# Optimization experiments

Hardware: AMD Instinct MI355X
Metric: run time of the kernel (lower is better)

Reference implementation:

```python
import jax, jax.numpy as jnp
import numpy as np

NEG_SLOPE = 0.2  # PyG GATConv default negative_slope
BN_EPS = 1e-5


def gat_layer(x, src, dst, W, b, a_src, a_dst, heads, out_ch, concat):
    # x: [N, Fin]; W: [Fin, heads*out_ch]; a_src/a_dst: [heads, out_ch]
    N = x.shape[0]
    h = (x @ W).reshape(N, heads, out_ch)
    s = (h * a_src).sum(-1)            # [N, H]
    d = (h * a_dst).sum(-1)            # [N, H]
    e = jax.nn.leaky_relu(s[src] + d[dst], NEG_SLOPE)   # [E, H]
    # segment softmax over incoming edges of each destination node
    m = jax.ops.segment_max(e, dst, num_segments=N)
    ex = jnp.exp(e - m[dst])
    denom = jax.ops.segment_sum(ex, dst, num_segments=N)
    alpha = ex / (denom[dst] + 1e-16)                   # [E, H]
    out = jax.ops.segment_sum(alpha[:, :, None] * h[src], dst, num_segments=N)  # [N,H,C]
    out = out.reshape(N, heads * out_ch) if concat else out.mean(axis=1)
    return out + b


def batchnorm(x, gamma, beta):
    mu = x.mean(axis=0)
    var = x.var(axis=0)
    return gamma * (x - mu) * jax.lax.rsqrt(var + BN_EPS) + beta


def setup_inputs() -> dict:
    key = jax.random.key(0)
    ks = jax.random.split(key, 24)
    N, E, Fin, Hd, heads, C = 50000, 800000, 128, 64, 4, 2
    wdim = Hd * heads  # 256
    inp = {
        'x': jax.random.normal(ks[0], (N, Fin), jnp.float32),
        'edge_index': jax.random.randint(ks[1], (2, E), 0, N, jnp.int64),
    }
    def glorot(k, shape):
        fan = shape[0] + shape[-1]
        return jax.random.normal(k, shape, jnp.float32) * np.sqrt(2.0 / fan)
    # layer 0: Fin -> heads x Hd (concat)
    inp['W0'] = glorot(ks[2], (Fin, wdim)); inp['b0'] = jnp.zeros((wdim,), jnp.float32)
    inp['asrc0'] = glorot(ks[3], (heads, Hd)); inp['adst0'] = glorot(ks[4], (heads, Hd))
    inp['g0'] = jnp.ones((wdim,), jnp.float32); inp['be0'] = jnp.zeros((wdim,), jnp.float32)
    # layer 1: wdim -> heads x Hd (concat)
    inp['W1'] = glorot(ks[5], (wdim, wdim)); inp['b1'] = jnp.zeros((wdim,), jnp.float32)
    inp['asrc1'] = glorot(ks[6], (heads, Hd)); inp['adst1'] = glorot(ks[7], (heads, Hd))
    inp['g1'] = jnp.ones((wdim,), jnp.float32); inp['be1'] = jnp.zeros((wdim,), jnp.float32)
    # layer 2: wdim -> 1 head x Hd (no concat)
    inp['W2'] = glorot(ks[8], (wdim, Hd)); inp['b2'] = jnp.zeros((Hd,), jnp.float32)
    inp['asrc2'] = glorot(ks[9], (1, Hd)); inp['adst2'] = glorot(ks[10], (1, Hd))
    inp['g2'] = jnp.ones((Hd,), jnp.float32); inp['be2'] = jnp.zeros((Hd,), jnp.float32)
    # classifier: Linear(2*Hd, Hd) -> ReLU -> Linear(Hd, C)
    inp['Wc1'] = glorot(ks[11], (2 * Hd, Hd)); inp['bc1'] = jnp.zeros((Hd,), jnp.float32)
    inp['Wc2'] = glorot(ks[12], (Hd, C)); inp['bc2'] = jnp.zeros((C,), jnp.float32)
    return inp


def reference(x, edge_index, W0, b0, asrc0, adst0, g0, be0,
              W1, b1, asrc1, adst1, g1, be1,
              W2, b2, asrc2, adst2, g2, be2,
              Wc1, bc1, Wc2, bc2):
    N = x.shape[0]
    # add self-loops (PyG GATConv default)
    loops = jnp.arange(N, dtype=edge_index.dtype)
    src = jnp.concatenate([edge_index[0], loops])
    dst = jnp.concatenate([edge_index[1], loops])
    heads, Hd = asrc0.shape[0], asrc0.shape[1]

    h = gat_layer(x, src, dst, W0, b0, asrc0, adst0, heads, Hd, True)
    h = jax.nn.relu(batchnorm(h, g0, be0))
    h = gat_layer(h, src, dst, W1, b1, asrc1, adst1, heads, Hd, True)
    h = jax.nn.relu(batchnorm(h, g1, be1))
    h = gat_layer(h, src, dst, W2, b2, asrc2, adst2, 1, Hd, False)
    h = jax.nn.relu(batchnorm(h, g2, be2))

    pooled = jnp.concatenate([h.mean(axis=0, keepdims=True),
                              h.max(axis=0, keepdims=True)], axis=1)  # [1, 2*Hd]
    z = jax.nn.relu(pooled @ Wc1 + bc1)
    return z @ Wc2 + bc2  # [1, num_classes]
```

## Files before the change

### kernel.cpp

```cpp
#include <hip/hip_runtime.h>


typedef unsigned int uint;
typedef unsigned short ushort;

#define NEG_SLOPE 0.2f
#define BN_EPS 1e-5f
#define NB_RED 256

typedef __attribute__((ext_vector_type(2))) float f32x2;

__device__ __forceinline__ float bf2f(uint u) { return __uint_as_float(u << 16); }
__device__ __forceinline__ ushort f2bf(float f) {
    uint u = __float_as_uint(f);
    u += 0x7fff + ((u >> 16) & 1);
    return (ushort)(u >> 16);
}


__global__ void prep_kernel(const float* __restrict__ x, ushort* __restrict__ xb,
                            int total_real, int total_pad,
                            const float* __restrict__ W0, ushort* __restrict__ w0t,
                            const float* __restrict__ W1, ushort* __restrict__ w1t,
                            const float* __restrict__ W2, ushort* __restrict__ w2t,
                            const int* __restrict__ ei, int* __restrict__ deg, int E) {
    int i = blockIdx.x * blockDim.x + threadIdx.x;
    if (i < total_pad) {
        xb[i] = (i < total_real) ? f2bf(x[i]) : (ushort)0;
        return;
    }
    int j = i - total_pad;
    if (j < 32768) {
        int n = j / 128, k = j - n * 128;
        w0t[j] = f2bf(W0[(size_t)k * 256 + n]);
        return;
    }
    j -= 32768;
    if (j < 65536) {
        int n = j / 256, k = j - n * 256;
        w1t[j] = f2bf(W1[(size_t)k * 256 + n]);
        return;
    }
    j -= 65536;
    if (j < 16384) {
        int n = j / 256, k = j - n * 256;
        w2t[j] = f2bf(W2[(size_t)k * 64 + n]);
        return;
    }
    j -= 16384;
    if (j < E) atomicAdd(&deg[ei[E + j]], 1);
}


__global__ void scan_part(const int* __restrict__ deg, int* __restrict__ offsets,
                          int* __restrict__ bsum, int N) {
    __shared__ int sh[256];
    int t = threadIdx.x;
    int base = blockIdx.x * 1024 + t * 4;
    int v0 = (base + 0 < N) ? deg[base + 0] : 0;
    int v1 = (base + 1 < N) ? deg[base + 1] : 0;
    int v2 = (base + 2 < N) ? deg[base + 2] : 0;
    int v3 = (base + 3 < N) ? deg[base + 3] : 0;
    int s = v0 + v1 + v2 + v3;
    sh[t] = s;
    __syncthreads();
    for (int off = 1; off < 256; off <<= 1) {
        int y = (t >= off) ? sh[t - off] : 0;
        __syncthreads();
        sh[t] += y;
        __syncthreads();
    }
    int p = sh[t] - s;
    if (base + 0 < N) offsets[base + 0] = p;
    p += v0;
    if (base + 1 < N) offsets[base + 1] = p;
    p += v1;
    if (base + 2 < N) offsets[base + 2] = p;
    p += v2;
    if (base + 3 < N) offsets[base + 3] = p;
    if (t == 255) bsum[blockIdx.x] = sh[255];
}

__global__ void scan_top(const int* __restrict__ bsum, int* __restrict__ bexcl,
                         int nb, int* __restrict__ offsets, int N) {
    if (threadIdx.x == 0) {
        int run = 0;
        for (int b = 0; b < nb; ++b) { bexcl[b] = run; run += bsum[b]; }
        offsets[N] = run;
    }
}

__global__ void scan_add(int* __restrict__ offsets, int* __restrict__ cursor,
                         const int* __restrict__ bexcl, int N) {
    int add = bexcl[blockIdx.x];
    int base = blockIdx.x * 1024 + threadIdx.x * 4;
#pragma unroll
    for (int k = 0; k < 4; ++k) {
        int i = base + k;
        if (i < N) { int v = offsets[i] + add; offsets[i] = v; cursor[i] = v; }
    }
}

__global__ void scatter_kernel(const int* __restrict__ ei, int* __restrict__ cursor,
                               int* __restrict__ srcs, int E) {
    int e = blockIdx.x * blockDim.x + threadIdx.x;
    if (e < E) {
        int s = ei[e];
        int d = ei[E + e];
        int p = atomicAdd(&cursor[d], 1);
        srcs[p] = s;
    }
}


typedef __attribute__((ext_vector_type(8))) short bf16x8;
typedef __attribute__((ext_vector_type(4))) float floatx4;

template <int BN, int H>
__launch_bounds__(256)
__global__ void mfma_gemm_bt(const ushort* __restrict__ A, const ushort* __restrict__ Bt,
                             ushort* __restrict__ C, const float* __restrict__ asrc,
                             const float* __restrict__ adst, float* __restrict__ sv,
                             float* __restrict__ dv, int K, int Nn) {
    constexpr int WCOLS = (BN == 128) ? 2 : 1;
    constexpr int WROWS = 4 / WCOLS;
    constexpr int MT = 128 / (WROWS * 16);
    constexpr int NT = BN / (WCOLS * 16);
    constexpr int BCALLS = (BN * 32 * 2) / 4096;

    __shared__ ushort As[128 * 32];
    __shared__ ushort Bs[BN * 32];

    int t = threadIdx.x;
    int w = t >> 6, l = t & 63;

    int rb, cb;
    if (BN == 128) {
        int nbr = (int)gridDim.x >> 1;
        int full = (nbr & ~7) << 1;
        int id = blockIdx.x;
        if (id < full) {
            rb = ((id >> 4) << 3) + (id & 7);
            cb = (id >> 3) & 1;
        } else {
            int o = id - full;
            int rem = nbr & 7;
            rb = (nbr & ~7) + (rem ? (o % rem) : 0);
            cb = rem ? (o / rem) : 0;
        }
    } else {
        rb = blockIdx.x;
        cb = 0;
    }
    int row0 = rb * 128;
    int col0 = cb * BN;
    int wr = (w / WCOLS) * (MT * 16);
    int wc = (w % WCOLS) * (NT * 16);

    floatx4 acc[MT][NT];
#pragma unroll
    for (int mi = 0; mi < MT; ++mi)
#pragma unroll
        for (int ni = 0; ni < NT; ++ni)
#pragma unroll
            for (int r = 0; r < 4; ++r) acc[mi][ni][r] = 0.f;

    int mrow = l & 15;
    int kc = (l >> 4) * 8;

    for (int kt = 0; kt < K; kt += 32) {
#pragma unroll
        for (int c = 0; c < 2; ++c) {
            int idx = c * 256 + t;
            const ushort* gp = A + (size_t)(row0 + (idx >> 2)) * K + kt + (idx & 3) * 8;
            __builtin_amdgcn_global_load_lds(
                (const __attribute__((address_space(1))) void*)gp,
                (__attribute__((address_space(3))) void*)(As + (idx & ~63) * 8),
                16, 0, 0);
        }
#pragma unroll
        for (int c = 0; c < BCALLS; ++c) {
            int idx = c * 256 + t;
            const ushort* gp = Bt + (size_t)(col0 + (idx >> 2)) * K + kt + (idx & 3) * 8;
            __builtin_amdgcn_global_load_lds(
                (const __attribute__((address_space(1))) void*)gp,
                (__attribute__((address_space(3))) void*)(Bs + (idx & ~63) * 8),
                16, 0, 0);
        }
        __syncthreads();

        bf16x8 af[MT], bfr[NT];
#pragma unroll
        for (int mi = 0; mi < MT; ++mi)
            af[mi] = *(const bf16x8*)&As[(wr + mi * 16 + mrow) * 32 + kc];
#pragma unroll
        for (int ni = 0; ni < NT; ++ni)
            bfr[ni] = *(const bf16x8*)&Bs[(wc + ni * 16 + mrow) * 32 + kc];
#pragma unroll
        for (int mi = 0; mi < MT; ++mi)
#pragma unroll
            for (int ni = 0; ni < NT; ++ni)
                acc[mi][ni] = __builtin_amdgcn_mfma_f32_16x16x32_bf16(
                    af[mi], bfr[ni], acc[mi][ni], 0, 0, 0);
        __syncthreads();
    }

#pragma unroll
    for (int mi = 0; mi < MT; ++mi) {
        int rbase = row0 + wr + mi * 16 + (l >> 4) * 4;
#pragma unroll
        for (int ni = 0; ni < NT; ++ni) {
            int col = col0 + wc + ni * 16 + (l & 15);
#pragma unroll
            for (int r = 0; r < 4; ++r)
                C[(size_t)(rbase + r) * Nn + col] = f2bf(acc[mi][ni][r]);
        }
    }

    float av[NT], bv[NT];
#pragma unroll
    for (int ni = 0; ni < NT; ++ni) {
        int ch = col0 + wc + ni * 16 + (l & 15);
        av[ni] = asrc[ch];
        bv[ni] = adst[ch];
    }
    int gh = (col0 + wc) >> 6;
#pragma unroll
    for (int mi = 0; mi < MT; ++mi) {
#pragma unroll
        for (int r = 0; r < 4; ++r) {
            float s = 0.f, d = 0.f;
#pragma unroll
            for (int ni = 0; ni < NT; ++ni) {
                float hv = acc[mi][ni][r];
                s += hv * av[ni];
                d += hv * bv[ni];
            }
#pragma unroll
            for (int m = 8; m >= 1; m >>= 1) {
                s += __shfl_xor(s, m);
                d += __shfl_xor(d, m);
            }
            if ((l & 15) == 0) {
                int row = row0 + wr + mi * 16 + (l >> 4) * 4 + r;
                sv[row * H + gh] = s;
                dv[row * H + gh] = d;
            }
        }
    }
}


#define CAP4 64

#define ACCUMW4(qv_, wt_) { \
    f32x2 wv_ = {(wt_), (wt_)}; \
    uint pr_[4] = {(qv_).x, (qv_).y, (qv_).z, (qv_).w}; \
    _Pragma("unroll") \
    for (int k_ = 0; k_ < 4; ++k_) { \
        f32x2 hv_ = {__uint_as_float(pr_[k_] << 16), \
                     __uint_as_float(pr_[k_] & 0xffff0000u)}; \
        ax[k_] += wv_ * hv_; \
    } }

#define LDQ4(kk_, wv_, qv_) { \
    int kq_ = (kk_); \
    if (kq_ < scnt) { \
        int nq_ = sidx[sub][kq_]; \
        wv_ = swgt[sub][kq_][head]; \
        qv_ = *(const uint4*)(hrow + (size_t)nq_ * 256); \
    } else { wv_ = 0.f; qv_.x = 0; qv_.y = 0; qv_.z = 0; qv_.w = 0; } }

__launch_bounds__(128)
__global__ void agg4_kernel(const ushort* __restrict__ hb, const float* __restrict__ sv,
                            const float* __restrict__ dv, const int* __restrict__ offsets,
                            const int* __restrict__ srcs, const float* __restrict__ bias,
                            ushort* __restrict__ zb, int N) {
    __shared__ int   sidx[4][CAP4];
    __shared__ float swgt[4][CAP4][4];
    __shared__ float lden[4][4];

    int t = threadIdx.x;
    int sub = t >> 5, gl = t & 31;
    int head = gl >> 3;
    int i = blockIdx.x * 4 + sub;
    bool valid = i < N;

    int beg = 0, cnt = 0;
    if (valid) { beg = offsets[i]; cnt = offsets[i + 1] - beg; }
    int scnt = cnt < CAP4 ? cnt : CAP4;

    if (gl < 4) lden[sub][gl] = 0.f;
    for (int k = gl; k < scnt; k += 32) sidx[sub][k] = srcs[beg + k];
    __syncthreads();

    {
        int h = gl & 3;
        float dvh = valid ? dv[i * 4 + h] : 0.f;
        float denp = 0.f;
        for (int idx = gl; idx < scnt * 4; idx += 32) {
            int k = idx >> 2;
            float e = sv[sidx[sub][k] * 4 + h] + dvh;
            float wgt = __expf(fminf(fmaxf(e, NEG_SLOPE * e), 60.f));
            swgt[sub][k][h] = wgt;
            denp += wgt;
        }
        atomicAdd(&lden[sub][h], denp);
    }
    __syncthreads();

    f32x2 ax[4] = {};
    const ushort* hrow = hb + gl * 8;

    float w0, w1, w2, w3;
    uint4 q0, q1, q2, q3;
    LDQ4(0, w0, q0); LDQ4(1, w1, q1); LDQ4(2, w2, q2); LDQ4(3, w3, q3);
    for (int k = 0; k < scnt; k += 4) {
        float v0 = w0, v1 = w1, v2 = w2, v3 = w3;
        uint4 p0 = q0, p1 = q1, p2 = q2, p3 = q3;
        LDQ4(k + 4, w0, q0); LDQ4(k + 5, w1, q1);
        LDQ4(k + 6, w2, q2); LDQ4(k + 7, w3, q3);
        ACCUMW4(p0, v0);
        ACCUMW4(p1, v1);
        ACCUMW4(p2, v2);
        ACCUMW4(p3, v3);
    }

    if (cnt > CAP4) {
        float d_i = dv[i * 4 + head];
        for (int k2 = CAP4; k2 < cnt; ++k2) {
            int n = srcs[beg + k2];
            float e = sv[n * 4 + head] + d_i;
            float wgt = __expf(fminf(fmaxf(e, NEG_SLOPE * e), 60.f));
            if ((gl & 7) == 0) atomicAdd(&lden[sub][head], wgt);
            uint4 q4 = *(const uint4*)(hrow + (size_t)n * 256);
            ACCUMW4(q4, wgt);
        }
    }

    if (valid) {
        float e_self = sv[i * 4 + head] + dv[i * 4 + head];
        float wself = __expf(fminf(fmaxf(e_self, NEG_SLOPE * e_self), 60.f));
        uint4 qs = *(const uint4*)&hb[(size_t)i * 256 + gl * 8];
        ACCUMW4(qs, wself);
        float rden = 1.f / (lden[sub][head] + wself + 1e-16f);
        const float* bb = bias + gl * 8;
        uint4 o;
        o.x = (uint)f2bf(ax[0].x * rden + bb[0]) | ((uint)f2bf(ax[0].y * rden + bb[1]) << 16);
        o.y = (uint)f2bf(ax[1].x * rden + bb[2]) | ((uint)f2bf(ax[1].y * rden + bb[3]) << 16);
        o.z = (uint)f2bf(ax[2].x * rden + bb[4]) | ((uint)f2bf(ax[2].y * rden + bb[5]) << 16);
        o.w = (uint)f2bf(ax[3].x * rden + bb[6]) | ((uint)f2bf(ax[3].y * rden + bb[7]) << 16);
        *(uint4*)&zb[(size_t)i * 256 + gl * 8] = o;
    }
}


#define CAP1 64

#define ACCUMW1(qv_, wt_) { \
    f32x2 wv_ = {(wt_), (wt_)}; \
    f32x2 h0_ = {__uint_as_float((qv_).x << 16), __uint_as_float((qv_).x & 0xffff0000u)}; \
    f32x2 h1_ = {__uint_as_float((qv_).y << 16), __uint_as_float((qv_).y & 0xffff0000u)}; \
    ax[0] += wv_ * h0_; \
    ax[1] += wv_ * h1_; }

#define LDQ1(kk_, wv_, qv_) { \
    int kq_ = (kk_); \
    if (kq_ < scnt) { \
        int nq_ = sidx[sub][kq_]; \
        wv_ = swgt[sub][kq_]; \
        qv_ = *(const uint2*)(hrow + (size_t)nq_ * 64); \
    } else { wv_ = 0.f; qv_.x = 0; qv_.y = 0; } }

__launch_bounds__(64)
__global__ void agg1_kernel(const ushort* __restrict__ hb, const float* __restrict__ sv,
                            const float* __restrict__ dv, const int* __restrict__ offsets,
                            const int* __restrict__ srcs, const float* __restrict__ bias,
                            ushort* __restrict__ zb, int N) {
    __shared__ int   sidx[4][CAP1];
    __shared__ float swgt[4][CAP1];
    __shared__ float lden[4];

    int t = threadIdx.x;
    int sub = t >> 4, gl = t & 15;
    int i = blockIdx.x * 4 + sub;
    bool valid = i < N;

    int beg = 0, cnt = 0;
    if (valid) { beg = offsets[i]; cnt = offsets[i + 1] - beg; }
    int scnt = cnt < CAP1 ? cnt : CAP1;

    if (gl == 0) lden[sub] = 0.f;
    for (int k = gl; k < scnt; k += 16) sidx[sub][k] = srcs[beg + k];
    __syncthreads();

    float d_i = valid ? dv[i] : 0.f;
    {
        float denp = 0.f;
        for (int k = gl; k < scnt; k += 16) {
            float e = sv[sidx[sub][k]] + d_i;
            float wgt = __expf(fminf(fmaxf(e, NEG_SLOPE * e), 60.f));
            swgt[sub][k] = wgt;
            denp += wgt;
        }
        atomicAdd(&lden[sub], denp);
    }
    __syncthreads();

    f32x2 ax[2] = {};
    const ushort* hrow = hb + gl * 4;

    float w0, w1, w2, w3;
    uint2 q0, q1, q2, q3;
    LDQ1(0, w0, q0); LDQ1(1, w1, q1); LDQ1(2, w2, q2); LDQ1(3, w3, q3);
    for (int k = 0; k < scnt; k += 4) {
        float v0 = w0, v1 = w1, v2 = w2, v3 = w3;
        uint2 p0 = q0, p1 = q1, p2 = q2, p3 = q3;
        LDQ1(k + 4, w0, q0); LDQ1(k + 5, w1, q1);
        LDQ1(k + 6, w2, q2); LDQ1(k + 7, w3, q3);
        ACCUMW1(p0, v0);
        ACCUMW1(p1, v1);
        ACCUMW1(p2, v2);
        ACCUMW1(p3, v3);
    }

    if (cnt > CAP1) {
        for (int k2 = CAP1; k2 < cnt; ++k2) {
            int n = srcs[beg + k2];
            float e = sv[n] + d_i;
            float wgt = __expf(fminf(fmaxf(e, NEG_SLOPE * e), 60.f));
            if (gl == 0) atomicAdd(&lden[sub], wgt);
            uint2 q2v = *(const uint2*)(hrow + (size_t)n * 64);
            ACCUMW1(q2v, wgt);
        }
    }

    if (valid) {
        float e_self = sv[i] + d_i;
        float wself = __expf(fminf(fmaxf(e_self, NEG_SLOPE * e_self), 60.f));
        uint2 qs = *(const uint2*)&hb[(size_t)i * 64 + gl * 4];
        ACCUMW1(qs, wself);
        float rden = 1.f / (lden[sub] + wself + 1e-16f);
        const float* bb = bias + gl * 4;
        uint2 o;
        o.x = (uint)f2bf(ax[0].x * rden + bb[0]) | ((uint)f2bf(ax[0].y * rden + bb[1]) << 16);
        o.y = (uint)f2bf(ax[1].x * rden + bb[2]) | ((uint)f2bf(ax[1].y * rden + bb[3]) << 16);
        *(uint2*)&zb[(size_t)i * 64 + gl * 4] = o;
    }
}


template <int F>
__launch_bounds__(256)
__global__ void bn_stats_kernel(const ushort* __restrict__ x, float* __restrict__ ps,
                                float* __restrict__ pq, int N) {
    constexpr int OCT = F / 8;
    __shared__ float lds_s[F], lds_q[F];
    int t = threadIdx.x;
    if (t < F) { lds_s[t] = 0.f; lds_q[t] = 0.f; }
    __syncthreads();

    float s[8] = {}, q[8] = {};
    int total8 = N * F / 8;
    for (int idx = blockIdx.x * 256 + t; idx < total8; idx += NB_RED * 256) {
        uint4 v = ((const uint4*)x)[idx];
        uint pr[4] = {v.x, v.y, v.z, v.w};
#pragma unroll
        for (int k = 0; k < 4; ++k) {
            float a = bf2f(pr[k] & 0xffffu);
            float b = bf2f(pr[k] >> 16);
            s[2 * k] += a;     q[2 * k] += a * a;
            s[2 * k + 1] += b; q[2 * k + 1] += b * b;
        }
    }
    int co = t % OCT;
#pragma unroll
    for (int j = 0; j < 8; ++j) {
        atomicAdd(&lds_s[co * 8 + j], s[j]);
        atomicAdd(&lds_q[co * 8 + j], q[j]);
    }
    __syncthreads();
    if (t < F) {
        ps[blockIdx.x * F + t] = lds_s[t];
        pq[blockIdx.x * F + t] = lds_q[t];
    }
}

__global__ void bn_final_kernel(const float* __restrict__ ps, const float* __restrict__ pq,
                                const float* __restrict__ g, const float* __restrict__ be,
                                float* __restrict__ scale, float* __restrict__ shift,
                                int N, int F) {
    int t = threadIdx.x;
    if (t < F) {
        float s = 0.f, q = 0.f;
        for (int b = 0; b < NB_RED; ++b) { s += ps[b * F + t]; q += pq[b * F + t]; }
        float mean = s / (float)N;
        float var = q / (float)N - mean * mean;
        float sc = g[t] * rsqrtf(var + BN_EPS);
        scale[t] = sc;
        shift[t] = be[t] - sc * mean;
    }
}

__global__ void bn_apply_kernel(uint* __restrict__ x, const float* __restrict__ scale,
                                const float* __restrict__ shift, int totalPairs, int Fmask) {
    int i = blockIdx.x * blockDim.x + threadIdx.x;
    if (i < totalPairs) {
        uint p = x[i];
        int c0 = (2 * i) & Fmask;
        float v0 = fmaxf(bf2f(p & 0xffffu) * scale[c0] + shift[c0], 0.f);
        float v1 = fmaxf(bf2f(p >> 16) * scale[c0 + 1] + shift[c0 + 1], 0.f);
        x[i] = (uint)f2bf(v0) | ((uint)f2bf(v1) << 16);
    }
}


__launch_bounds__(256)
__global__ void pool_kernel(const ushort* __restrict__ y, const float* __restrict__ scale,
                            const float* __restrict__ shift, float* __restrict__ psum,
                            float* __restrict__ pmax, int N) {
    constexpr int F = 64, OCT = 8;
    __shared__ float lds_s[F];
    __shared__ uint lds_m[F];
    int t = threadIdx.x;
    if (t < F) { lds_s[t] = 0.f; lds_m[t] = 0u; }
    __syncthreads();

    int co = t % OCT;
    float sc[8], sh[8];
#pragma unroll
    for (int j = 0; j < 8; ++j) { sc[j] = scale[co * 8 + j]; sh[j] = shift[co * 8 + j]; }

    float s[8] = {}, m[8] = {};
    int total8 = N * F / 8;
    for (int idx = blockIdx.x * 256 + t; idx < total8; idx += NB_RED * 256) {
        uint4 v = ((const uint4*)y)[idx];
        uint pr[4] = {v.x, v.y, v.z, v.w};
#pragma unroll
        for (int k = 0; k < 4; ++k) {
            float a = fmaxf(bf2f(pr[k] & 0xffffu) * sc[2 * k] + sh[2 * k], 0.f);
            float b = fmaxf(bf2f(pr[k] >> 16) * sc[2 * k + 1] + sh[2 * k + 1], 0.f);
            s[2 * k] += a;     m[2 * k] = fmaxf(m[2 * k], a);
            s[2 * k + 1] += b; m[2 * k + 1] = fmaxf(m[2 * k + 1], b);
        }
    }
#pragma unroll
    for (int j = 0; j < 8; ++j) {
        atomicAdd(&lds_s[co * 8 + j], s[j]);
        atomicMax(&lds_m[co * 8 + j], __float_as_uint(m[j]));
    }
    __syncthreads();
    if (t < F) {
        psum[blockIdx.x * F + t] = lds_s[t];
        pmax[blockIdx.x * F + t] = __uint_as_float(lds_m[t]);
    }
}

__global__ void classify_kernel(const float* __restrict__ psum, const float* __restrict__ pmax,
                                const float* __restrict__ Wc1, const float* __restrict__ bc1,
                                const float* __restrict__ Wc2, const float* __restrict__ bc2,
                                float* __restrict__ out, int N) {
    __shared__ float pooled[128];
    __shared__ float z[64];
    int t = threadIdx.x;
    if (t < 64) {
        float s = 0.f;
        for (int b = 0; b < NB_RED; ++b) s += psum[b * 64 + t];
        pooled[t] = s / (float)N;
    } else {
        int c = t - 64;
        float m = 0.f;
        for (int b = 0; b < NB_RED; ++b) m = fmaxf(m, pmax[b * 64 + c]);
        pooled[t] = m;
    }
    __syncthreads();
    if (t < 64) {
        float a = bc1[t];
        for (int k = 0; k < 128; ++k) a += pooled[k] * Wc1[k * 64 + t];
        z[t] = a > 0.f ? a : 0.f;
    }
    __syncthreads();
    if (t < 2) {
        float a = bc2[t];
        for (int j = 0; j < 64; ++j) a += z[j] * Wc2[j * 2 + t];
        out[t] = a;
    }
}


extern "C" void kernel_launch(void* const* d_in, const int* in_sizes, int n_in,
                              void* d_out, int out_size, void* d_ws, size_t ws_size,
                              hipStream_t stream) {
    const float* x   = (const float*)d_in[0];
    const int*   ei  = (const int*)d_in[1];
    const float* W0  = (const float*)d_in[2];  const float* b0  = (const float*)d_in[3];
    const float* as0 = (const float*)d_in[4];  const float* ad0 = (const float*)d_in[5];
    const float* g0  = (const float*)d_in[6];  const float* be0 = (const float*)d_in[7];
    const float* W1  = (const float*)d_in[8];  const float* b1  = (const float*)d_in[9];
    const float* as1 = (const float*)d_in[10]; const float* ad1 = (const float*)d_in[11];
    const float* g1  = (const float*)d_in[12]; const float* be1 = (const float*)d_in[13];
    const float* W2  = (const float*)d_in[14]; const float* b2  = (const float*)d_in[15];
    const float* as2 = (const float*)d_in[16]; const float* ad2 = (const float*)d_in[17];
    const float* g2  = (const float*)d_in[18]; const float* be2 = (const float*)d_in[19];
    const float* Wc1 = (const float*)d_in[20]; const float* bc1 = (const float*)d_in[21];
    const float* Wc2 = (const float*)d_in[22]; const float* bc2 = (const float*)d_in[23];
    float* out = (float*)d_out;

    const int N = in_sizes[0] / 128;
    const int E = in_sizes[1] / 2;
    const int Mpad = ((N + 127) / 128) * 128;
    const int NB_SCAN = (N + 1023) / 1024;
    const int NBROW = Mpad / 128;
    const int NB_AGG = (N + 3) / 4;

    char* ws = (char*)d_ws;
    size_t o = 0;
    auto alloc = [&](size_t bytes) -> void* {
        void* p = ws + o;
        o = (o + bytes + 255) & ~(size_t)255;
        return p;
    };
    int*    deg     = (int*)alloc((size_t)N * 4);
    int*    offsets = (int*)alloc((size_t)(N + 1) * 4);
    int*    cursor  = (int*)alloc((size_t)N * 4);
    int*    srcs    = (int*)alloc((size_t)E * 4);
    int*    bsum    = (int*)alloc((size_t)NB_SCAN * 4);
    int*    bexcl   = (int*)alloc((size_t)NB_SCAN * 4);
    ushort* xb      = (ushort*)alloc((size_t)Mpad * 128 * 2);
    ushort* w0t     = (ushort*)alloc((size_t)256 * 128 * 2);
    ushort* w1t     = (ushort*)alloc((size_t)256 * 256 * 2);
    ushort* w2t     = (ushort*)alloc((size_t)64 * 256 * 2);
    ushort* hb      = (ushort*)alloc((size_t)Mpad * 256 * 2);
    ushort* zb      = (ushort*)alloc((size_t)Mpad * 256 * 2);
    float*  sv      = (float*)alloc((size_t)Mpad * 4 * 4);
    float*  dv      = (float*)alloc((size_t)Mpad * 4 * 4);
    float*  ps      = (float*)alloc((size_t)NB_RED * 256 * 4);
    float*  pq      = (float*)alloc((size_t)NB_RED * 256 * 4);
    float*  scale   = (float*)alloc(256 * 4);
    float*  shift   = (float*)alloc(256 * 4);
    float*  psum    = (float*)alloc((size_t)NB_RED * 64 * 4);
    float*  pmax    = (float*)alloc((size_t)NB_RED * 64 * 4);

    (void)hipMemsetAsync(deg, 0, (size_t)N * 4, stream);
    int prep_total = Mpad * 128 + 32768 + 65536 + 16384 + E;
    prep_kernel<<<(prep_total + 255) / 256, 256, 0, stream>>>(
        x, xb, N * 128, Mpad * 128, W0, w0t, W1, w1t, W2, w2t, ei, deg, E);

    scan_part<<<NB_SCAN, 256, 0, stream>>>(deg, offsets, bsum, N);
    scan_top<<<1, 64, 0, stream>>>(bsum, bexcl, NB_SCAN, offsets, N);
    scan_add<<<NB_SCAN, 256, 0, stream>>>(offsets, cursor, bexcl, N);
    scatter_kernel<<<(E + 255) / 256, 256, 0, stream>>>(ei, cursor, srcs, E);

    {
        mfma_gemm_bt<128, 4><<<NBROW * 2, 256, 0, stream>>>(xb, w0t, hb, as0, ad0, sv, dv, 128, 256);
        agg4_kernel<<<NB_AGG, 128, 0, stream>>>(hb, sv, dv, offsets, srcs, b0, zb, N);
        bn_stats_kernel<256><<<NB_RED, 256, 0, stream>>>(zb, ps, pq, N);
        bn_final_kernel<<<1, 256, 0, stream>>>(ps, pq, g0, be0, scale, shift, N, 256);
        bn_apply_kernel<<<(N * 128 + 255) / 256, 256, 0, stream>>>((uint*)zb, scale, shift,
                                                                   N * 128, 255);
    }
    {
        mfma_gemm_bt<128, 4><<<NBROW * 2, 256, 0, stream>>>(zb, w1t, hb, as1, ad1, sv, dv, 256, 256);
        agg4_kernel<<<NB_AGG, 128, 0, stream>>>(hb, sv, dv, offsets, srcs, b1, zb, N);
        bn_stats_kernel<256><<<NB_RED, 256, 0, stream>>>(zb, ps, pq, N);
        bn_final_kernel<<<1, 256, 0, stream>>>(ps, pq, g1, be1, scale, shift, N, 256);
        bn_apply_kernel<<<(N * 128 + 255) / 256, 256, 0, stream>>>((uint*)zb, scale, shift,
                                                                   N * 128, 255);
    }
    {
        mfma_gemm_bt<64, 1><<<NBROW, 256, 0, stream>>>(zb, w2t, hb, as2, ad2, sv, dv, 256, 64);
        agg1_kernel<<<NB_AGG, 64, 0, stream>>>(hb, sv, dv, offsets, srcs, b2, zb, N);
        bn_stats_kernel<64><<<NB_RED, 256, 0, stream>>>(zb, ps, pq, N);
        bn_final_kernel<<<1, 64, 0, stream>>>(ps, pq, g2, be2, scale, shift, N, 64);
    }

    pool_kernel<<<NB_RED, 256, 0, stream>>>(zb, scale, shift, psum, pmax, N);
    classify_kernel<<<1, 128, 0, stream>>>(psum, pmax, Wc1, bc1, Wc2, bc2, out, N);
}
```

Baseline: 588.1 us.

## Store GEMM output in column-chunked layout and split aggregation by channel chunk

The GEMM now writes its hidden features into a column-blocked layout: 32-channel chunks for the 4-head layers and 8-channel chunks for the last layer, each stored contiguously across all rows. The aggregation kernels launch 8 blocks per group of 8 nodes, one per channel chunk, so each block gathers a narrow slice whose total working set is smaller and more cache-resident. Each thread group splits the edge list across lanes and combines partial sums with shuffles, replacing the LDS atomics. The cost is that attention weights are recomputed once per chunk, and the GEMM stores become more strided.

```diff
diff --git a/kernel.cpp b/kernel.cpp
--- a/kernel.cpp
+++ b/kernel.cpp
@@ -121,12 +121,14 @@
 __global__ void mfma_gemm_bt(const ushort* __restrict__ A, const ushort* __restrict__ Bt,
                              ushort* __restrict__ C, const float* __restrict__ asrc,
                              const float* __restrict__ adst, float* __restrict__ sv,
-                             float* __restrict__ dv, int K, int Nn) {
+                             float* __restrict__ dv, int K, int Nn, int Mpad) {
     constexpr int WCOLS = (BN == 128) ? 2 : 1;
     constexpr int WROWS = 4 / WCOLS;
     constexpr int MT = 128 / (WROWS * 16);
     constexpr int NT = BN / (WCOLS * 16);
     constexpr int BCALLS = (BN * 32 * 2) / 4096;
+    constexpr int SCH = (BN == 64) ? 8 : 32;
+    constexpr int SSH = (BN == 64) ? 3 : 5;
 
     __shared__ ushort As[128 * 32];
     __shared__ ushort Bs[BN * 32];
@@ -211,9 +213,10 @@
 #pragma unroll
         for (int ni = 0; ni < NT; ++ni) {
             int col = col0 + wc + ni * 16 + (l & 15);
+            size_t sb = ((size_t)(col >> SSH) * Mpad) * SCH + (col & (SCH - 1));
 #pragma unroll
             for (int r = 0; r < 4; ++r)
-                C[(size_t)(rbase + r) * Nn + col] = f2bf(acc[mi][ni][r]);
+                C[sb + (size_t)(rbase + r) * SCH] = f2bf(acc[mi][ni][r]);
         }
     }
 
@@ -267,185 +270,168 @@
     int kq_ = (kk_); \
     if (kq_ < scnt) { \
         int nq_ = sidx[sub][kq_]; \
-        wv_ = swgt[sub][kq_][head]; \
-        qv_ = *(const uint4*)(hrow + (size_t)nq_ * 256); \
+        wv_ = swgt[sub][kq_]; \
+        qv_ = *(const uint4*)(gbase + (size_t)nq_ * 32); \
     } else { wv_ = 0.f; qv_.x = 0; qv_.y = 0; qv_.z = 0; qv_.w = 0; } }
 
 __launch_bounds__(128)
-__global__ void agg4_kernel(const ushort* __restrict__ hb, const float* __restrict__ sv,
+__global__ void agg4_kernel(const ushort* __restrict__ hbT, const float* __restrict__ sv,
                             const float* __restrict__ dv, const int* __restrict__ offsets,
                             const int* __restrict__ srcs, const float* __restrict__ bias,
-                            ushort* __restrict__ zb, int N) {
-    __shared__ int   sidx[4][CAP4];
-    __shared__ float swgt[4][CAP4][4];
-    __shared__ float lden[4][4];
-
-    int t = threadIdx.x;
-    int sub = t >> 5, gl = t & 31;
-    int head = gl >> 3;
-    int i = blockIdx.x * 4 + sub;
+                            ushort* __restrict__ zb, int N, int Mpad) {
+    __shared__ int   sidx[8][CAP4];
+    __shared__ float swgt[8][CAP4];
+
+    int t = threadIdx.x;
+    int sub = t >> 4, gl = t & 15;
+    int bid = blockIdx.x;
+    int c = bid & 7;
+    int head = c >> 1;
+    int i = (bid >> 3) * 8 + sub;
     bool valid = i < N;
 
     int beg = 0, cnt = 0;
     if (valid) { beg = offsets[i]; cnt = offsets[i + 1] - beg; }
     int scnt = cnt < CAP4 ? cnt : CAP4;
 
-    if (gl < 4) lden[sub][gl] = 0.f;
-    for (int k = gl; k < scnt; k += 32) sidx[sub][k] = srcs[beg + k];
-    __syncthreads();
-
-    {
-        int h = gl & 3;
-        float dvh = valid ? dv[i * 4 + h] : 0.f;
-        float denp = 0.f;
-        for (int idx = gl; idx < scnt * 4; idx += 32) {
-            int k = idx >> 2;
-            float e = sv[sidx[sub][k] * 4 + h] + dvh;
-            float wgt = __expf(fminf(fmaxf(e, NEG_SLOPE * e), 60.f));
-            swgt[sub][k][h] = wgt;
-            denp += wgt;
-        }
-        atomicAdd(&lden[sub][h], denp);
-    }
+    for (int k = gl; k < scnt; k += 16) sidx[sub][k] = srcs[beg + k];
+    __syncthreads();
+
+    float dvh = valid ? dv[i * 4 + head] : 0.f;
+    float den = 0.f;
+    for (int k = gl; k < scnt; k += 16) {
+        float e = sv[sidx[sub][k] * 4 + head] + dvh;
+        float wgt = __expf(fminf(fmaxf(e, NEG_SLOPE * e), 60.f));
+        swgt[sub][k] = wgt;
+        den += wgt;
+    }
+    den += __shfl_xor(den, 1);
+    den += __shfl_xor(den, 2);
+    den += __shfl_xor(den, 4);
+    den += __shfl_xor(den, 8);
     __syncthreads();
 
     f32x2 ax[4] = {};
-    const ushort* hrow = hb + gl * 8;
-
-    float w0, w1, w2, w3;
-    uint4 q0, q1, q2, q3;
-    LDQ4(0, w0, q0); LDQ4(1, w1, q1); LDQ4(2, w2, q2); LDQ4(3, w3, q3);
-    for (int k = 0; k < scnt; k += 4) {
-        float v0 = w0, v1 = w1, v2 = w2, v3 = w3;
-        uint4 p0 = q0, p1 = q1, p2 = q2, p3 = q3;
-        LDQ4(k + 4, w0, q0); LDQ4(k + 5, w1, q1);
-        LDQ4(k + 6, w2, q2); LDQ4(k + 7, w3, q3);
+    int chunk = gl & 3;
+    int esub = gl >> 2;
+    const ushort* gbase = hbT + (size_t)c * Mpad * 32 + chunk * 8;
+
+    float wA, wB;
+    uint4 qA, qB;
+    LDQ4(esub, wA, qA);
+    LDQ4(esub + 4, wB, qB);
+    for (int k = esub; k < scnt; k += 8) {
+        float v0 = wA, v1 = wB;
+        uint4 p0 = qA, p1 = qB;
+        LDQ4(k + 8, wA, qA);
+        LDQ4(k + 12, wB, qB);
         ACCUMW4(p0, v0);
         ACCUMW4(p1, v1);
-        ACCUMW4(p2, v2);
-        ACCUMW4(p3, v3);
     }
 
     if (cnt > CAP4) {
-        float d_i = dv[i * 4 + head];
-        for (int k2 = CAP4; k2 < cnt; ++k2) {
+        float dslow = 0.f;
+        for (int k2 = CAP4 + esub; k2 < cnt; k2 += 4) {
             int n = srcs[beg + k2];
-            float e = sv[n * 4 + head] + d_i;
+            float e = sv[n * 4 + head] + dvh;
             float wgt = __expf(fminf(fmaxf(e, NEG_SLOPE * e), 60.f));
-            if ((gl & 7) == 0) atomicAdd(&lden[sub][head], wgt);
-            uint4 q4 = *(const uint4*)(hrow + (size_t)n * 256);
+            if (chunk == 0) dslow += wgt;
+            uint4 q4 = *(const uint4*)(gbase + (size_t)n * 32);
             ACCUMW4(q4, wgt);
         }
-    }
-
-    if (valid) {
-        float e_self = sv[i * 4 + head] + dv[i * 4 + head];
+        dslow += __shfl_xor(dslow, 1);
+        dslow += __shfl_xor(dslow, 2);
+        dslow += __shfl_xor(dslow, 4);
+        dslow += __shfl_xor(dslow, 8);
+        den += dslow;
+    }
+
+#pragma unroll
+    for (int j = 0; j < 4; ++j) {
+        ax[j].x += __shfl_xor(ax[j].x, 4);
+        ax[j].y += __shfl_xor(ax[j].y, 4);
+        ax[j].x += __shfl_xor(ax[j].x, 8);
+        ax[j].y += __shfl_xor(ax[j].y, 8);
+    }
+
+    if (valid && esub == 0) {
+        float e_self = sv[i * 4 + head] + dvh;
         float wself = __expf(fminf(fmaxf(e_self, NEG_SLOPE * e_self), 60.f));
-        uint4 qs = *(const uint4*)&hb[(size_t)i * 256 + gl * 8];
+        uint4 qs = *(const uint4*)(gbase + (size_t)i * 32);
         ACCUMW4(qs, wself);
-        float rden = 1.f / (lden[sub][head] + wself + 1e-16f);
-        const float* bb = bias + gl * 8;
+        float rden = 1.f / (den + wself + 1e-16f);
+        const float* bb = bias + c * 32 + chunk * 8;
         uint4 o;
         o.x = (uint)f2bf(ax[0].x * rden + bb[0]) | ((uint)f2bf(ax[0].y * rden + bb[1]) << 16);
         o.y = (uint)f2bf(ax[1].x * rden + bb[2]) | ((uint)f2bf(ax[1].y * rden + bb[3]) << 16);
         o.z = (uint)f2bf(ax[2].x * rden + bb[4]) | ((uint)f2bf(ax[2].y * rden + bb[5]) << 16);
         o.w = (uint)f2bf(ax[3].x * rden + bb[6]) | ((uint)f2bf(ax[3].y * rden + bb[7]) << 16);
-        *(uint4*)&zb[(size_t)i * 256 + gl * 8] = o;
-    }
-}
-
-
-#define CAP1 64
-
-#define ACCUMW1(qv_, wt_) { \
-    f32x2 wv_ = {(wt_), (wt_)}; \
-    f32x2 h0_ = {__uint_as_float((qv_).x << 16), __uint_as_float((qv_).x & 0xffff0000u)}; \
-    f32x2 h1_ = {__uint_as_float((qv_).y << 16), __uint_as_float((qv_).y & 0xffff0000u)}; \
-    ax[0] += wv_ * h0_; \
-    ax[1] += wv_ * h1_; }
-
-#define LDQ1(kk_, wv_, qv_) { \
-    int kq_ = (kk_); \
-    if (kq_ < scnt) { \
-        int nq_ = sidx[sub][kq_]; \
-        wv_ = swgt[sub][kq_]; \
-        qv_ = *(const uint2*)(hrow + (size_t)nq_ * 64); \
-    } else { wv_ = 0.f; qv_.x = 0; qv_.y = 0; } }
+        *(uint4*)&zb[(size_t)i * 256 + c * 32 + chunk * 8] = o;
+    }
+}
+
 
 __launch_bounds__(64)
-__global__ void agg1_kernel(const ushort* __restrict__ hb, const float* __restrict__ sv,
+__global__ void agg1_kernel(const ushort* __restrict__ hbT, const float* __restrict__ sv,
                             const float* __restrict__ dv, const int* __restrict__ offsets,
                             const int* __restrict__ srcs, const float* __restrict__ bias,
-                            ushort* __restrict__ zb, int N) {
-    __shared__ int   sidx[4][CAP1];
-    __shared__ float swgt[4][CAP1];
-    __shared__ float lden[4];
-
-    int t = threadIdx.x;
-    int sub = t >> 4, gl = t & 15;
-    int i = blockIdx.x * 4 + sub;
+                            ushort* __restrict__ zb, int N, int Mpad) {
+    int t = threadIdx.x;
+    int sub = t >> 3, gl = t & 7;
+    int bid = blockIdx.x;
+    int c = bid & 7;
+    int i = (bid >> 3) * 8 + sub;
     bool valid = i < N;
 
     int beg = 0, cnt = 0;
     if (valid) { beg = offsets[i]; cnt = offsets[i + 1] - beg; }
-    int scnt = cnt < CAP1 ? cnt : CAP1;
-
-    if (gl == 0) lden[sub] = 0.f;
-    for (int k = gl; k < scnt; k += 16) sidx[sub][k] = srcs[beg + k];
-    __syncthreads();
 
     float d_i = valid ? dv[i] : 0.f;
-    {
-        float denp = 0.f;
-        for (int k = gl; k < scnt; k += 16) {
-            float e = sv[sidx[sub][k]] + d_i;
-            float wgt = __expf(fminf(fmaxf(e, NEG_SLOPE * e), 60.f));
-            swgt[sub][k] = wgt;
-            denp += wgt;
-        }
-        atomicAdd(&lden[sub], denp);
-    }
-    __syncthreads();
-
-    f32x2 ax[2] = {};
-    const ushort* hrow = hb + gl * 4;
-
-    float w0, w1, w2, w3;
-    uint2 q0, q1, q2, q3;
-    LDQ1(0, w0, q0); LDQ1(1, w1, q1); LDQ1(2, w2, q2); LDQ1(3, w3, q3);
-    for (int k = 0; k < scnt; k += 4) {
-        float v0 = w0, v1 = w1, v2 = w2, v3 = w3;
-        uint2 p0 = q0, p1 = q1, p2 = q2, p3 = q3;
-        LDQ1(k + 4, w0, q0); LDQ1(k + 5, w1, q1);
-        LDQ1(k + 6, w2, q2); LDQ1(k + 7, w3, q3);
-        ACCUMW1(p0, v0);
-        ACCUMW1(p1, v1);
-        ACCUMW1(p2, v2);
-        ACCUMW1(p3, v3);
-    }
-
-    if (cnt > CAP1) {
-        for (int k2 = CAP1; k2 < cnt; ++k2) {
-            int n = srcs[beg + k2];
-            float e = sv[n] + d_i;
-            float wgt = __expf(fminf(fmaxf(e, NEG_SLOPE * e), 60.f));
-            if (gl == 0) atomicAdd(&lden[sub], wgt);
-            uint2 q2v = *(const uint2*)(hrow + (size_t)n * 64);
-            ACCUMW1(q2v, wgt);
-        }
-    }
-
-    if (valid) {
+    const ushort* gbase = hbT + (size_t)c * Mpad * 8;
+
+    f32x2 ax[4] = {};
+    float den = 0.f;
+
+    int k = gl;
+    int nA = (k < cnt) ? srcs[beg + k] : 0;
+    while (k < cnt) {
+        int kn = k + 8;
+        int nB = (kn < cnt) ? srcs[beg + kn] : 0;
+        float s = sv[nA];
+        uint4 q = *(const uint4*)(gbase + (size_t)nA * 8);
+        float e = s + d_i;
+        float wgt = __expf(fminf(fmaxf(e, NEG_SLOPE * e), 60.f));
+        den += wgt;
+        ACCUMW4(q, wgt);
+        k = kn; nA = nB;
+    }
+
+    den += __shfl_xor(den, 1);
+    den += __shfl_xor(den, 2);
+    den += __shfl_xor(den, 4);
+#pragma unroll
+    for (int j = 0; j < 4; ++j) {
+        ax[j].x += __shfl_xor(ax[j].x, 1);
+        ax[j].y += __shfl_xor(ax[j].y, 1);
+        ax[j].x += __shfl_xor(ax[j].x, 2);
+        ax[j].y += __shfl_xor(ax[j].y, 2);
+        ax[j].x += __shfl_xor(ax[j].x, 4);
+        ax[j].y += __shfl_xor(ax[j].y, 4);
+    }
+
+    if (valid && gl == 0) {
         float e_self = sv[i] + d_i;
         float wself = __expf(fminf(fmaxf(e_self, NEG_SLOPE * e_self), 60.f));
-        uint2 qs = *(const uint2*)&hb[(size_t)i * 64 + gl * 4];
-        ACCUMW1(qs, wself);
-        float rden = 1.f / (lden[sub] + wself + 1e-16f);
-        const float* bb = bias + gl * 4;
-        uint2 o;
+        uint4 qs = *(const uint4*)(gbase + (size_t)i * 8);
+        ACCUMW4(qs, wself);
+        float rden = 1.f / (den + wself + 1e-16f);
+        const float* bb = bias + c * 8;
+        uint4 o;
         o.x = (uint)f2bf(ax[0].x * rden + bb[0]) | ((uint)f2bf(ax[0].y * rden + bb[1]) << 16);
         o.y = (uint)f2bf(ax[1].x * rden + bb[2]) | ((uint)f2bf(ax[1].y * rden + bb[3]) << 16);
-        *(uint2*)&zb[(size_t)i * 64 + gl * 4] = o;
+        o.z = (uint)f2bf(ax[2].x * rden + bb[4]) | ((uint)f2bf(ax[2].y * rden + bb[5]) << 16);
+        o.w = (uint)f2bf(ax[3].x * rden + bb[6]) | ((uint)f2bf(ax[3].y * rden + bb[7]) << 16);
+        *(uint4*)&zb[(size_t)i * 64 + c * 8] = o;
     }
 }
 
@@ -611,7 +597,7 @@
     const int Mpad = ((N + 127) / 128) * 128;
     const int NB_SCAN = (N + 1023) / 1024;
     const int NBROW = Mpad / 128;
-    const int NB_AGG = (N + 3) / 4;
+    const int NB_AGG = ((N + 7) / 8) * 8;
 
     char* ws = (char*)d_ws;
     size_t o = 0;
@@ -652,24 +638,27 @@
     scatter_kernel<<<(E + 255) / 256, 256, 0, stream>>>(ei, cursor, srcs, E);
 
     {
-        mfma_gemm_bt<128, 4><<<NBROW * 2, 256, 0, stream>>>(xb, w0t, hb, as0, ad0, sv, dv, 128, 256);
-        agg4_kernel<<<NB_AGG, 128, 0, stream>>>(hb, sv, dv, offsets, srcs, b0, zb, N);
+        mfma_gemm_bt<128, 4><<<NBROW * 2, 256, 0, stream>>>(xb, w0t, hb, as0, ad0, sv, dv,
+                                                            128, 256, Mpad);
+        agg4_kernel<<<NB_AGG, 128, 0, stream>>>(hb, sv, dv, offsets, srcs, b0, zb, N, Mpad);
         bn_stats_kernel<256><<<NB_RED, 256, 0, stream>>>(zb, ps, pq, N);
         bn_final_kernel<<<1, 256, 0, stream>>>(ps, pq, g0, be0, scale, shift, N, 256);
         bn_apply_kernel<<<(N * 128 + 255) / 256, 256, 0, stream>>>((uint*)zb, scale, shift,
                                                                    N * 128, 255);
     }
     {
-        mfma_gemm_bt<128, 4><<<NBROW * 2, 256, 0, stream>>>(zb, w1t, hb, as1, ad1, sv, dv, 256, 256);
-        agg4_kernel<<<NB_AGG, 128, 0, stream>>>(hb, sv, dv, offsets, srcs, b1, zb, N);
+        mfma_gemm_bt<128, 4><<<NBROW * 2, 256, 0, stream>>>(zb, w1t, hb, as1, ad1, sv, dv,
+                                                            256, 256, Mpad);
+        agg4_kernel<<<NB_AGG, 128, 0, stream>>>(hb, sv, dv, offsets, srcs, b1, zb, N, Mpad);
         bn_stats_kernel<256><<<NB_RED, 256, 0, stream>>>(zb, ps, pq, N);
         bn_final_kernel<<<1, 256, 0, stream>>>(ps, pq, g1, be1, scale, shift, N, 256);
         bn_apply_kernel<<<(N * 128 + 255) / 256, 256, 0, stream>>>((uint*)zb, scale, shift,
                                                                    N * 128, 255);
     }
     {
-        mfma_gemm_bt<64, 1><<<NBROW, 256, 0, stream>>>(zb, w2t, hb, as2, ad2, sv, dv, 256, 64);
-        agg1_kernel<<<NB_AGG, 64, 0, stream>>>(hb, sv, dv, offsets, srcs, b2, zb, N);
+        mfma_gemm_bt<64, 1><<<NBROW, 256, 0, stream>>>(zb, w2t, hb, as2, ad2, sv, dv,
+                                                       256, 64, Mpad);
+        agg1_kernel<<<NB_AGG, 64, 0, stream>>>(hb, sv, dv, offsets, srcs, b2, zb, N, Mpad);
         bn_stats_kernel<64><<<NB_RED, 256, 0, stream>>>(zb, ps, pq, N);
         bn_final_kernel<<<1, 64, 0, stream>>>(ps, pq, g2, be2, scale, shift, N, 64);
     }
```

Result: slower. 651.6 us (+10.8%).
